# Performance work log

Hardware: AMD Instinct MI355X
Metric: run time of the kernel (lower is better)

## Reference

```python
import jax, jax.numpy as jnp
import numpy as np

N = 50000      # nodes
E = 800000     # edges (avg degree 16)
HID = 64       # hidden_dim
NH = 4         # heads
HC = HID // NH # channels per head = 16
EMB = 8        # emb_dim
EDIM = 6       # edge_dim
SDIM = 6       # state_dim
FEAT = 7       # raw node feature width
NSENS = 3


def setup_inputs() -> dict:
    key = jax.random.key(0)
    k = jax.random.split(key, 32)
    s = 0.1
    p = {}
    p['x'] = jax.random.normal(k[0], (N, FEAT), jnp.float32)
    p['node_type'] = jax.random.randint(k[1], (N,), 0, 2)
    p['sensor_id'] = jax.random.randint(k[2], (N,), 0, NSENS + 1)
    p['edge_index'] = jax.random.randint(k[3], (2, E), 0, N)
    p['edge_attr'] = jax.random.normal(k[4], (E, EDIM), jnp.float32)
    p['hidden_state'] = jnp.zeros((N, HID), jnp.float32)
    # embeddings
    p['type_emb'] = jax.random.normal(k[5], (2, EMB)) * s
    p['sensor_emb'] = jax.random.normal(k[6], (NSENS + 1, EMB)) * s
    # encoder MLP
    p['enc_w1'] = jax.random.normal(k[7], (FEAT + 2 * EMB, HID)) * s
    p['enc_b1'] = jnp.zeros((HID,))
    p['enc_w2'] = jax.random.normal(k[8], (HID, HID)) * s
    p['enc_b2'] = jnp.zeros((HID,))
    # GATv2 layer 1 (lin_l, lin_r with bias; lin_edge no bias; att [NH,HC]; out bias)
    p['g1_wl'] = jax.random.normal(k[9], (HID, HID)) * s
    p['g1_bl'] = jnp.zeros((HID,))
    p['g1_wr'] = jax.random.normal(k[10], (HID, HID)) * s
    p['g1_br'] = jnp.zeros((HID,))
    p['g1_we'] = jax.random.normal(k[11], (EDIM, HID)) * s
    p['g1_att'] = jax.random.normal(k[12], (NH, HC)) * s
    p['g1_bias'] = jnp.zeros((HID,))
    # GATv2 layer 2
    p['g2_wl'] = jax.random.normal(k[13], (HID, HID)) * s
    p['g2_bl'] = jnp.zeros((HID,))
    p['g2_wr'] = jax.random.normal(k[14], (HID, HID)) * s
    p['g2_br'] = jnp.zeros((HID,))
    p['g2_we'] = jax.random.normal(k[15], (EDIM, HID)) * s
    p['g2_att'] = jax.random.normal(k[16], (NH, HC)) * s
    p['g2_bias'] = jnp.zeros((HID,))
    # GRUCell (torch layout transposed: [in, 3*hid], gate order r,z,n)
    p['gru_wih'] = jax.random.normal(k[17], (HID, 3 * HID)) * s
    p['gru_bih'] = jnp.zeros((3 * HID,))
    p['gru_whh'] = jax.random.normal(k[18], (HID, 3 * HID)) * s
    p['gru_bhh'] = jnp.zeros((3 * HID,))
    # decoder MLP
    p['dec_w1'] = jax.random.normal(k[19], (HID, HID)) * s
    p['dec_b1'] = jnp.zeros((HID,))
    p['dec_w2'] = jax.random.normal(k[20], (HID, SDIM + 1)) * s
    p['dec_b2'] = jnp.zeros((SDIM + 1,))
    return p


def _gatv2(h, src, dst, edge_attr, wl, bl, wr, br, we, att, bias):
    # PyG GATv2Conv, concat=True, negative_slope=0.2, edge_dim features
    xl = (h @ wl + bl).reshape(-1, NH, HC)  # source transform [N,H,C]
    xr = (h @ wr + br).reshape(-1, NH, HC)  # target transform [N,H,C]
    xe = (edge_attr @ we).reshape(-1, NH, HC)  # edge transform [E,H,C]
    m = jax.nn.leaky_relu(xl[src] + xr[dst] + xe, 0.2)  # [E,H,C]
    logits = jnp.einsum('ehc,hc->eh', m, att)  # [E,H]
    # scatter-softmax over incoming edges of each destination node
    mx = jax.ops.segment_max(logits, dst, num_segments=N)
    ex = jnp.exp(logits - mx[dst])
    den = jax.ops.segment_sum(ex, dst, num_segments=N)
    alpha = ex / (den[dst] + 1e-16)  # [E,H]
    out = jax.ops.segment_sum(xl[src] * alpha[:, :, None], dst, num_segments=N)
    return out.reshape(-1, NH * HC) + bias, alpha


def reference(x, node_type, sensor_id, edge_index, edge_attr, hidden_state,
              type_emb, sensor_emb, enc_w1, enc_b1, enc_w2, enc_b2,
              g1_wl, g1_bl, g1_wr, g1_br, g1_we, g1_att, g1_bias,
              g2_wl, g2_bl, g2_wr, g2_br, g2_we, g2_att, g2_bias,
              gru_wih, gru_bih, gru_whh, gru_bhh,
              dec_w1, dec_b1, dec_w2, dec_b2):
    src, dst = edge_index[0], edge_index[1]
    h = jnp.concatenate([x, type_emb[node_type], sensor_emb[sensor_id]], axis=-1)
    h = jax.nn.relu(h @ enc_w1 + enc_b1) @ enc_w2 + enc_b2
    h, alpha1 = _gatv2(h, src, dst, edge_attr, g1_wl, g1_bl, g1_wr, g1_br, g1_we, g1_att, g1_bias)
    h = jax.nn.relu(h)
    h, alpha2 = _gatv2(h, src, dst, edge_attr, g2_wl, g2_bl, g2_wr, g2_br, g2_we, g2_att, g2_bias)
    # GRUCell (torch gate order: r, z, n)
    gi = h @ gru_wih + gru_bih
    gh = hidden_state @ gru_whh + gru_bhh
    r = jax.nn.sigmoid(gi[:, :HID] + gh[:, :HID])
    z = jax.nn.sigmoid(gi[:, HID:2 * HID] + gh[:, HID:2 * HID])
    n = jnp.tanh(gi[:, 2 * HID:] + r * gh[:, 2 * HID:])
    new_hidden = (1.0 - z) * n + z * hidden_state
    out = jax.nn.relu(new_hidden @ dec_w1 + dec_b1) @ dec_w2 + dec_b2
    return out, new_hidden, alpha1, alpha2
```

## Files before the change

kernel.cpp:

```cpp
#include <hip/hip_runtime.h>
#include <hip/hip_bf16.h>

static constexpr int N_ = 50000;
static constexpr int E_ = 800000;
static constexpr int CAP = 128;


#define GEMM_FMA_BLOCK(AV, W0, W1, ROW)                                              \
      acc[ROW][0]=fmaf(AV,W0.x,acc[ROW][0]); acc[ROW][1]=fmaf(AV,W0.y,acc[ROW][1]);  \
      acc[ROW][2]=fmaf(AV,W0.z,acc[ROW][2]); acc[ROW][3]=fmaf(AV,W0.w,acc[ROW][3]);  \
      acc[ROW][4]=fmaf(AV,W1.x,acc[ROW][4]); acc[ROW][5]=fmaf(AV,W1.y,acc[ROW][5]);  \
      acc[ROW][6]=fmaf(AV,W1.z,acc[ROW][6]); acc[ROW][7]=fmaf(AV,W1.w,acc[ROW][7]);

#define GEMM_KLOOP(KQc)                                                              \
  _Pragma("unroll 1")                                                                \
  for (int kg = 0; kg < (KQc); ++kg) {                                               \
    float4 a0 = At4[kg * 129 + rowb];                                                \
    float4 a1 = At4[kg * 129 + rowb + 32];                                           \
    float4 a2 = At4[kg * 129 + rowb + 64];                                           \
    float4 a3 = At4[kg * 129 + rowb + 96];                                           \
    _Pragma("unroll")                                                                \
    for (int t = 0; t < 4; ++t) {                                                    \
      float4 w0 = *(const float4*)(Wt + (kg * 4 + t) * 64 + j0);                     \
      float4 w1 = *(const float4*)(Wt + (kg * 4 + t) * 64 + j0 + 4);                 \
      float av0 = t==0?a0.x:t==1?a0.y:t==2?a0.z:a0.w;                                \
      float av1 = t==0?a1.x:t==1?a1.y:t==2?a1.z:a1.w;                                \
      float av2 = t==0?a2.x:t==1?a2.y:t==2?a2.z:a2.w;                                \
      float av3 = t==0?a3.x:t==1?a3.y:t==2?a3.z:a3.w;                                \
      GEMM_FMA_BLOCK(av0, w0, w1, 0)                                                 \
      GEMM_FMA_BLOCK(av1, w0, w1, 1)                                                 \
      GEMM_FMA_BLOCK(av2, w0, w1, 2)                                                 \
      GEMM_FMA_BLOCK(av3, w0, w1, 3)                                                 \
    }                                                                                \
  }

#define ACC_INIT(BPTR)                                                               \
  {                                                                                  \
    float4 b0v = *(const float4*)((BPTR) + j0);                                      \
    float4 b1v = *(const float4*)((BPTR) + j0 + 4);                                  \
    _Pragma("unroll")                                                                \
    for (int i = 0; i < 4; ++i) {                                                    \
      acc[i][0]=b0v.x; acc[i][1]=b0v.y; acc[i][2]=b0v.z; acc[i][3]=b0v.w;            \
      acc[i][4]=b1v.x; acc[i][5]=b1v.y; acc[i][6]=b1v.z; acc[i][7]=b1v.w;            \
    }                                                                                \
  }

#define STAGE_W(WPTR, LDW, KPADc, KREAL)                                             \
  for (int idx = tid; idx < (KPADc) * 16; idx += 256) {                              \
    int k = idx >> 4, jq = idx & 15;                                                 \
    float4 v = (k < (KREAL)) ? *(const float4*)((WPTR) + (size_t)k * (LDW) + jq * 4) \
                             : make_float4(0.f, 0.f, 0.f, 0.f);                      \
    *(float4*)(Wt + k * 64 + jq * 4) = v;                                            \
  }

#define STAGE_A(APTR, LDA, KQc)                                                      \
  for (int idx = tid; idx < 128 * (KQc); idx += 256) {                               \
    int r = idx / (KQc), kq = idx - r * (KQc);                                       \
    int node = nb + r;                                                               \
    float4 v = (node < N_) ? *(const float4*)((APTR) + (size_t)node * (LDA) + kq * 4)\
                           : make_float4(0.f, 0.f, 0.f, 0.f);                        \
    At4[kq * 129 + r] = v;                                                           \
  }

#define STORE_C(CPTR, LDC, RELUc, ACCc)                                              \
  _Pragma("unroll")                                                                  \
  for (int i = 0; i < 4; ++i) {                                                      \
    int node = nb + rowb + 32 * i;                                                   \
    if (node < N_) {                                                                 \
      float* cp = (CPTR) + (size_t)node * (LDC) + j0;                                \
      float o0=acc[i][0],o1=acc[i][1],o2=acc[i][2],o3=acc[i][3];                     \
      float o4=acc[i][4],o5=acc[i][5],o6=acc[i][6],o7=acc[i][7];                     \
      if (RELUc) { o0=fmaxf(o0,0.f);o1=fmaxf(o1,0.f);o2=fmaxf(o2,0.f);o3=fmaxf(o3,0.f); \
                   o4=fmaxf(o4,0.f);o5=fmaxf(o5,0.f);o6=fmaxf(o6,0.f);o7=fmaxf(o7,0.f); } \
      if (ACCc) { float4 c0=*(const float4*)cp; float4 c1=*(const float4*)(cp+4);    \
                  o0+=c0.x;o1+=c0.y;o2+=c0.z;o3+=c0.w;o4+=c1.x;o5+=c1.y;o6+=c1.z;o7+=c1.w; } \
      *(float4*)cp = make_float4(o0,o1,o2,o3);                                       \
      *(float4*)(cp+4) = make_float4(o4,o5,o6,o7);                                   \
    }                                                                                \
  }

__global__ void k_hist(const int* __restrict__ ei, int* __restrict__ deg) {
  int e = blockIdx.x * blockDim.x + threadIdx.x;
  if (e < E_) atomicAdd(&deg[ei[E_ + e]], 1);
}

__global__ __launch_bounds__(1024) void k_scan_blk(const int* __restrict__ deg,
                                                   int* __restrict__ off,
                                                   int* __restrict__ bsum) {
  __shared__ int sm[1024];
  int t = threadIdx.x;
  int i = blockIdx.x * 1024 + t;
  int v = (i < N_) ? deg[i] : 0;
  sm[t] = v;
  __syncthreads();
  for (int s = 1; s < 1024; s <<= 1) {
    int u = (t >= s) ? sm[t - s] : 0;
    __syncthreads();
    sm[t] += u;
    __syncthreads();
  }
  if (i < N_) off[i] = sm[t] - v;
  if (t == 1023) bsum[blockIdx.x] = sm[t];
}

__global__ void k_scan_top(int* __restrict__ bsum, int nb) {
  int t = threadIdx.x;
  int v = (t < nb) ? bsum[t] : 0;
  int orig = v;
  for (int s = 1; s < 64; s <<= 1) {
    int u = __shfl_up(v, s);
    if (t >= s) v += u;
  }
  if (t < nb) bsum[t] = v - orig;
}

__global__ void k_scan_add(int* __restrict__ off, const int* __restrict__ bsum,
                           int* __restrict__ cur) {
  int i = blockIdx.x * blockDim.x + threadIdx.x;
  if (i < N_) {
    int o = off[i] + bsum[i >> 10];
    off[i] = o;
    cur[i] = o;
  }
  if (i == 0) off[N_] = E_;
}

__global__ void k_scatter(const int* __restrict__ ei, int* __restrict__ cursor,
                          int2* __restrict__ csr_es) {
  int e = blockIdx.x * blockDim.x + threadIdx.x;
  if (e < E_) {
    int s = ei[e];
    int d = ei[E_ + e];
    int p = atomicAdd(&cursor[d], 1);
    csr_es[p] = make_int2(e, s);
  }
}

__device__ __forceinline__ float encval(int c, int node, int nt, int sd,
                                        const float* __restrict__ x,
                                        const float* __restrict__ temb,
                                        const float* __restrict__ semb) {
  if (c < 7) return x[node * 7 + c];
  if (c < 15) return temb[nt * 8 + c - 7];
  if (c < 23) return semb[sd * 8 + c - 15];
  return 0.f;
}

__global__ __launch_bounds__(256, 3) void k_gemm_enc(
    const float* __restrict__ x, const int* __restrict__ ntype, const int* __restrict__ sid,
    const float* __restrict__ temb, const float* __restrict__ semb,
    const float* __restrict__ w1, const float* __restrict__ b1,
    float* __restrict__ hout) {
  __shared__ float4 At4[6 * 129];
  __shared__ float Wt[24 * 64];
  int tid = threadIdx.x;
  int nb = blockIdx.x * 128;
  for (int idx = tid; idx < 128 * 6; idx += 256) {
    int r = idx / 6, kq = idx - r * 6;
    int node = nb + r;
    float v0 = 0.f, v1 = 0.f, v2 = 0.f, v3 = 0.f;
    if (node < N_) {
      int nt = ntype[node], sd = sid[node];
      int c = kq * 4;
      v0 = encval(c, node, nt, sd, x, temb, semb);
      v1 = encval(c + 1, node, nt, sd, x, temb, semb);
      v2 = encval(c + 2, node, nt, sd, x, temb, semb);
      v3 = encval(c + 3, node, nt, sd, x, temb, semb);
    }
    At4[kq * 129 + r] = make_float4(v0, v1, v2, v3);
  }
  STAGE_W(w1, 64, 24, 23)
  __syncthreads();
  int col = tid & 7, rowb = tid >> 3;
  int j0 = col * 8;
  float acc[4][8];
  ACC_INIT(b1)
  GEMM_KLOOP(6)
  STORE_C(hout, 64, true, false)
}

__global__ __launch_bounds__(256, 3) void k_gemm64(
    const float* __restrict__ A, const float* __restrict__ W,
    const float* __restrict__ bias, float* __restrict__ C) {
  __shared__ float4 At4[16 * 129];
  __shared__ float Wt[64 * 64];
  int tid = threadIdx.x;
  int nb = blockIdx.x * 128;
  STAGE_A(A, 64, 16)
  STAGE_W(W, 64, 64, 64)
  __syncthreads();
  int col = tid & 7, rowb = tid >> 3;
  int j0 = col * 8;
  float acc[4][8];
  ACC_INIT(bias)
  GEMM_KLOOP(16)
  STORE_C(C, 64, false, false)
}

__global__ __launch_bounds__(256, 3) void k_gemm2(
    const float* __restrict__ A,
    const float* __restrict__ Wl, const float* __restrict__ bl,
    const float* __restrict__ Wr, const float* __restrict__ br,
    float* __restrict__ Cl, float* __restrict__ Cr) {
  __shared__ float4 At4[16 * 129];
  __shared__ float Wt[64 * 64];
  int tid = threadIdx.x;
  int nb = blockIdx.x * 128;
  const float* W = blockIdx.y ? Wr : Wl;
  const float* b = blockIdx.y ? br : bl;
  float* C       = blockIdx.y ? Cr : Cl;
  STAGE_A(A, 64, 16)
  STAGE_W(W, 64, 64, 64)
  __syncthreads();
  int col = tid & 7, rowb = tid >> 3;
  int j0 = col * 8;
  float acc[4][8];
  ACC_INIT(b)
  GEMM_KLOOP(16)
  STORE_C(C, 64, false, false)
}

__global__ __launch_bounds__(256, 3) void k_gru_ih(
    const float* __restrict__ A,
    const float* __restrict__ wih, const float* __restrict__ bih,
    float* __restrict__ gbuf) {
  __shared__ float4 At4[16 * 129];
  __shared__ float Wt[64 * 64];
  int tid = threadIdx.x;
  int nb = blockIdx.x * 128;
  int ch = blockIdx.y;
  int col = tid & 7, rowb = tid >> 3;
  int j0 = col * 8;
  STAGE_A(A, 64, 16)
  STAGE_W(wih + ch * 64, 192, 64, 64)
  __syncthreads();
  float acc[4][8];
  ACC_INIT(bih + ch * 64)
  GEMM_KLOOP(16)
  STORE_C(gbuf + ch * 64, 192, false, false)
}

__global__ __launch_bounds__(256, 3) void k_gru_hh(
    const float* __restrict__ hs,
    const float* __restrict__ whh, const float* __restrict__ bhh,
    float* __restrict__ gbuf, float* __restrict__ outnh) {
  __shared__ float4 At4[16 * 129];
  __shared__ float Wt[64 * 64];
  int tid = threadIdx.x;
  int nb = blockIdx.x * 128;
  int col = tid & 7, rowb = tid >> 3;
  int j0 = col * 8;
  STAGE_A(hs, 64, 16)
  float acc[4][8];
  for (int ch = 0; ch < 3; ++ch) {
    __syncthreads();
    STAGE_W(whh + ch * 64, 192, 64, 64)
    __syncthreads();
    ACC_INIT(bhh + ch * 64)
    GEMM_KLOOP(16)
    if (ch < 2) { STORE_C(gbuf + ch * 64, 192, false, true) }
  }
#define GATE1(RU, ZU, NU, SU, AU, OUT)                                   \
  { float rr = 1.f / (1.f + __expf(-(RU)));                              \
    float zz = 1.f / (1.f + __expf(-(ZU)));                              \
    float nn = tanhf((NU) + rr * (AU));                                  \
    OUT = (1.f - zz) * nn + zz * (SU); }
#pragma unroll
  for (int i = 0; i < 4; ++i) {
    int node = nb + rowb + 32 * i;
    if (node < N_) {
      const float* gp = gbuf + (size_t)node * 192;
      float4 r0 = *(const float4*)(gp + j0);
      float4 r1 = *(const float4*)(gp + j0 + 4);
      float4 z0 = *(const float4*)(gp + 64 + j0);
      float4 z1 = *(const float4*)(gp + 64 + j0 + 4);
      float4 n0 = *(const float4*)(gp + 128 + j0);
      float4 n1 = *(const float4*)(gp + 128 + j0 + 4);
      float4 s0 = *(const float4*)(hs + (size_t)node * 64 + j0);
      float4 s1 = *(const float4*)(hs + (size_t)node * 64 + j0 + 4);
      float q0, q1, q2, q3, q4, q5, q6, q7;
      GATE1(r0.x, z0.x, n0.x, s0.x, acc[i][0], q0)
      GATE1(r0.y, z0.y, n0.y, s0.y, acc[i][1], q1)
      GATE1(r0.z, z0.z, n0.z, s0.z, acc[i][2], q2)
      GATE1(r0.w, z0.w, n0.w, s0.w, acc[i][3], q3)
      GATE1(r1.x, z1.x, n1.x, s1.x, acc[i][4], q4)
      GATE1(r1.y, z1.y, n1.y, s1.y, acc[i][5], q5)
      GATE1(r1.z, z1.z, n1.z, s1.z, acc[i][6], q6)
      GATE1(r1.w, z1.w, n1.w, s1.w, acc[i][7], q7)
      float* op = outnh + (size_t)node * 64 + j0;
      *(float4*)op = make_float4(q0, q1, q2, q3);
      *(float4*)(op + 4) = make_float4(q4, q5, q6, q7);
    }
  }
#undef GATE1
}

__global__ __launch_bounds__(256, 3) void k_dec(
    const float* __restrict__ A,
    const float* __restrict__ w1, const float* __restrict__ b1,
    const float* __restrict__ w2, const float* __restrict__ b2,
    float* __restrict__ out) {
  __shared__ __align__(16) float pool[8320];
  __shared__ float Wt[64 * 64];
  float4* At4 = (float4*)pool;
  float* dtile = pool;
  int tid = threadIdx.x;
  int nb = blockIdx.x * 128;
  STAGE_A(A, 64, 16)
  STAGE_W(w1, 64, 64, 64)
  __syncthreads();
  int col = tid & 7, rowb = tid >> 3;
  int j0 = col * 8;
  float acc[4][8];
  ACC_INIT(b1)
  GEMM_KLOOP(16)
  __syncthreads();
#pragma unroll
  for (int i = 0; i < 4; ++i) {
    int rl = rowb + 32 * i;
#pragma unroll
    for (int u = 0; u < 8; ++u) dtile[rl * 65 + j0 + u] = fmaxf(acc[i][u], 0.f);
  }
  __syncthreads();
  if (tid < 128) {
    int node = nb + tid;
    if (node < N_) {
      float o0 = b2[0], o1 = b2[1], o2 = b2[2], o3 = b2[3], o4 = b2[4], o5 = b2[5], o6 = b2[6];
#pragma unroll 1
      for (int k = 0; k < 64; ++k) {
        float xv = dtile[tid * 65 + k];
        o0 = fmaf(xv, w2[k * 7 + 0], o0);
        o1 = fmaf(xv, w2[k * 7 + 1], o1);
        o2 = fmaf(xv, w2[k * 7 + 2], o2);
        o3 = fmaf(xv, w2[k * 7 + 3], o3);
        o4 = fmaf(xv, w2[k * 7 + 4], o4);
        o5 = fmaf(xv, w2[k * 7 + 5], o5);
        o6 = fmaf(xv, w2[k * 7 + 6], o6);
      }
      float* op = out + (size_t)node * 7;
      op[0] = o0; op[1] = o1; op[2] = o2; op[3] = o3; op[4] = o4; op[5] = o5; op[6] = o6;
    }
  }
}

template <bool RELU>
__global__ __launch_bounds__(64, 6) void k_fused(
    const int* __restrict__ off, const int2* __restrict__ csr_es,
    const float* __restrict__ eattr,
    const float* __restrict__ xl, const float* __restrict__ xr,
    const float* __restrict__ we, const float* __restrict__ att,
    const float* __restrict__ bias,
    float* __restrict__ hout, float* __restrict__ alpha) {
  __shared__ float wes[6 * 64];
  __shared__ float exbuf[CAP * 4];
  __shared__ int ebuf[CAP];
  int lane = threadIdx.x & 63;
  int slot = lane >> 4;
  int q = lane & 15;
  int head = q >> 2;
  int sb = slot << 4;
  int v = blockIdx.x;

#pragma unroll
  for (int i = 0; i < 6; ++i) wes[i * 64 + lane] = we[i * 64 + lane];

  int p0 = off[v], p1 = off[v + 1];
  int cnt = p1 - p0;

  float att4[4], b4[4];
#pragma unroll
  for (int r = 0; r < 4; ++r) { att4[r] = att[q * 4 + r]; b4[r] = bias[q * 4 + r]; }

  float4 xr4 = *(const float4*)(xr + (size_t)v * 64 + q * 4);
  float num0 = 0.f, num1 = 0.f, num2 = 0.f, num3 = 0.f, den = 0.f;

  __syncthreads();

  int p = p0 + slot;
  int2 es = (p < p1) ? csr_es[p] : make_int2(0, 0);
  for (int base = 0; base < cnt; base += 4) {
    bool valid = (p0 + base + slot) < p1;
    int e = es.x, s = es.y;
    int pn = p0 + base + 4 + slot;
    int2 esn = (pn < p1) ? csr_es[pn] : make_int2(0, 0);
    float ea = (valid && q < 6) ? eattr[(size_t)e * 6 + q] : 0.f;
    float4 xls = valid ? *(const float4*)(xl + (size_t)s * 64 + q * 4)
                       : make_float4(0.f, 0.f, 0.f, 0.f);
    float m0 = xls.x + xr4.x, m1 = xls.y + xr4.y, m2 = xls.z + xr4.z, m3 = xls.w + xr4.w;
#pragma unroll
    for (int i = 0; i < 6; ++i) {
      float eai = __shfl(ea, sb + i);
      float4 w4 = *(const float4*)(wes + i * 64 + q * 4);
      m0 = fmaf(eai, w4.x, m0);
      m1 = fmaf(eai, w4.y, m1);
      m2 = fmaf(eai, w4.z, m2);
      m3 = fmaf(eai, w4.w, m3);
    }
    m0 = (m0 > 0.f) ? m0 : 0.2f * m0;
    m1 = (m1 > 0.f) ? m1 : 0.2f * m1;
    m2 = (m2 > 0.f) ? m2 : 0.2f * m2;
    m3 = (m3 > 0.f) ? m3 : 0.2f * m3;
    float t = m0 * att4[0];
    t = fmaf(m1, att4[1], t);
    t = fmaf(m2, att4[2], t);
    t = fmaf(m3, att4[3], t);
    t += __shfl_xor(t, 1);
    t += __shfl_xor(t, 2);
    float ex = valid ? __expf(t) : 0.f;
    den += ex;
    num0 = fmaf(xls.x, ex, num0);
    num1 = fmaf(xls.y, ex, num1);
    num2 = fmaf(xls.z, ex, num2);
    num3 = fmaf(xls.w, ex, num3);
    int idx = base + slot;
    if (valid && idx < CAP) {
      if ((lane & 3) == 0) exbuf[idx * 4 + head] = ex;
      if (q == 0) ebuf[idx] = e;
    }
    es = esn;
  }
  num0 += __shfl_xor(num0, 16); num0 += __shfl_xor(num0, 32);
  num1 += __shfl_xor(num1, 16); num1 += __shfl_xor(num1, 32);
  num2 += __shfl_xor(num2, 16); num2 += __shfl_xor(num2, 32);
  num3 += __shfl_xor(num3, 16); num3 += __shfl_xor(num3, 32);
  den  += __shfl_xor(den, 16);  den  += __shfl_xor(den, 32);
  float dinv = 1.f / (den + 1e-16f);
  float o0 = fmaf(num0, dinv, b4[0]);
  float o1 = fmaf(num1, dinv, b4[1]);
  float o2 = fmaf(num2, dinv, b4[2]);
  float o3 = fmaf(num3, dinv, b4[3]);
  if (RELU) {
    o0 = fmaxf(o0, 0.f); o1 = fmaxf(o1, 0.f); o2 = fmaxf(o2, 0.f); o3 = fmaxf(o3, 0.f);
  }
  if (slot == 0)
    *(float4*)(hout + (size_t)v * 64 + q * 4) = make_float4(o0, o1, o2, o3);
  float dh = __shfl(dinv, (lane & 3) << 2);
  if (cnt <= CAP) {
    for (int base2 = 0; base2 < cnt; base2 += 16) {
      int idx = base2 + (lane >> 2);
      if (idx < cnt) {
        float exv = exbuf[idx * 4 + (lane & 3)];
        int e = ebuf[idx];
        alpha[(size_t)e * 4 + (lane & 3)] = exv * dh;
      }
    }
  } else {
    for (int pp = p0; pp < p1; ++pp) {
      int2 es2 = csr_es[pp];
      int e = es2.x, s = es2.y;
      float ea = (q < 6) ? eattr[(size_t)e * 6 + q] : 0.f;
      float4 xls = *(const float4*)(xl + (size_t)s * 64 + q * 4);
      float m0 = xls.x + xr4.x, m1 = xls.y + xr4.y, m2 = xls.z + xr4.z, m3 = xls.w + xr4.w;
#pragma unroll
      for (int i = 0; i < 6; ++i) {
        float eai = __shfl(ea, i);
        float4 w4 = *(const float4*)(wes + i * 64 + q * 4);
        m0 = fmaf(eai, w4.x, m0);
        m1 = fmaf(eai, w4.y, m1);
        m2 = fmaf(eai, w4.z, m2);
        m3 = fmaf(eai, w4.w, m3);
      }
      m0 = (m0 > 0.f) ? m0 : 0.2f * m0;
      m1 = (m1 > 0.f) ? m1 : 0.2f * m1;
      m2 = (m2 > 0.f) ? m2 : 0.2f * m2;
      m3 = (m3 > 0.f) ? m3 : 0.2f * m3;
      float t = m0 * att4[0];
      t = fmaf(m1, att4[1], t);
      t = fmaf(m2, att4[2], t);
      t = fmaf(m3, att4[3], t);
      t += __shfl_xor(t, 1);
      t += __shfl_xor(t, 2);
      if (slot == 0 && (lane & 3) == 0)
        alpha[(size_t)e * 4 + head] = __expf(t) * dinv;
    }
  }
}

extern "C" void kernel_launch(void* const* d_in, const int* in_sizes, int n_in,
                              void* d_out, int out_size, void* d_ws, size_t ws_size,
                              hipStream_t stream) {
  const float* x      = (const float*)d_in[0];
  const int* ntype    = (const int*)d_in[1];
  const int* sid      = (const int*)d_in[2];
  const int* ei       = (const int*)d_in[3];
  const float* eattr  = (const float*)d_in[4];
  const float* hs     = (const float*)d_in[5];
  const float* temb   = (const float*)d_in[6];
  const float* semb   = (const float*)d_in[7];
  const float* enc_w1 = (const float*)d_in[8];
  const float* enc_b1 = (const float*)d_in[9];
  const float* enc_w2 = (const float*)d_in[10];
  const float* enc_b2 = (const float*)d_in[11];
  const float* g1_wl  = (const float*)d_in[12];
  const float* g1_bl  = (const float*)d_in[13];
  const float* g1_wr  = (const float*)d_in[14];
  const float* g1_br  = (const float*)d_in[15];
  const float* g1_we  = (const float*)d_in[16];
  const float* g1_att = (const float*)d_in[17];
  const float* g1_bias= (const float*)d_in[18];
  const float* g2_wl  = (const float*)d_in[19];
  const float* g2_bl  = (const float*)d_in[20];
  const float* g2_wr  = (const float*)d_in[21];
  const float* g2_br  = (const float*)d_in[22];
  const float* g2_we  = (const float*)d_in[23];
  const float* g2_att = (const float*)d_in[24];
  const float* g2_bias= (const float*)d_in[25];
  const float* gru_wih= (const float*)d_in[26];
  const float* gru_bih= (const float*)d_in[27];
  const float* gru_whh= (const float*)d_in[28];
  const float* gru_bhh= (const float*)d_in[29];
  const float* dec_w1 = (const float*)d_in[30];
  const float* dec_b1 = (const float*)d_in[31];
  const float* dec_w2 = (const float*)d_in[32];
  const float* dec_b2 = (const float*)d_in[33];

  float* ws = (float*)d_ws;
  float* hA = ws;
  float* hB = hA + N_ * 64;
  float* xl = hB + N_ * 64;
  float* xr = xl + N_ * 64;
  float* U  = xr + N_ * 64;
  int* deg  = (int*)(U + N_ * 64);
  int* off  = deg + N_;
  int* cur  = off + N_ + 1;
  int* bsum = cur + N_;
  int2* csr_es = (int2*)(bsum + 64);

  float* gbuf = hB;

  float* out0  = (float*)d_out;
  float* outnh = out0 + N_ * 7;
  float* outa1 = outnh + N_ * 64;
  float* outa2 = outa1 + E_ * 4;

  const int NB_SCAN = (N_ + 1023) / 1024;
  const int NB_GEMM = (N_ + 127) / 128;

  hipMemsetAsync(deg, 0, N_ * sizeof(int), stream);
  k_hist<<<(E_ + 255) / 256, 256, 0, stream>>>(ei, deg);
  k_scan_blk<<<NB_SCAN, 1024, 0, stream>>>(deg, off, bsum);
  k_scan_top<<<1, 64, 0, stream>>>(bsum, NB_SCAN);
  k_scan_add<<<(N_ + 255) / 256, 256, 0, stream>>>(off, bsum, cur);
  k_scatter<<<(E_ + 255) / 256, 256, 0, stream>>>(ei, cur, csr_es);

  k_gemm_enc<<<NB_GEMM, 256, 0, stream>>>(x, ntype, sid, temb, semb, enc_w1, enc_b1, hB);
  k_gemm64<<<NB_GEMM, 256, 0, stream>>>(hB, enc_w2, enc_b2, hA);
  k_gemm2<<<dim3(NB_GEMM, 2), 256, 0, stream>>>(hA, g1_wl, g1_bl, g1_wr, g1_br, xl, xr);
  k_fused<true><<<N_, 64, 0, stream>>>(off, csr_es, eattr, xl, xr,
                                       g1_we, g1_att, g1_bias, hB, outa1);
  k_gemm2<<<dim3(NB_GEMM, 2), 256, 0, stream>>>(hB, g2_wl, g2_bl, g2_wr, g2_br, xl, xr);
  k_fused<false><<<N_, 64, 0, stream>>>(off, csr_es, eattr, xl, xr,
                                        g2_we, g2_att, g2_bias, hA, outa2);
  k_gru_ih<<<dim3(NB_GEMM, 3), 256, 0, stream>>>(hA, gru_wih, gru_bih, gbuf);
  k_gru_hh<<<NB_GEMM, 256, 0, stream>>>(hs, gru_whh, gru_bhh, gbuf, outnh);
  k_dec<<<NB_GEMM, 256, 0, stream>>>(outnh, dec_w1, dec_b1, dec_w2, dec_b2, out0);
}
```

Baseline: 529.0 us.

## Fuse encoder GEMMs and GRU GEMMs, unroll edge loop by two, nontemporal alpha stores

The two encoder GEMMs are merged into one kernel that keeps the ReLU intermediate in shared memory, and the two GRU kernels are merged so the gate preactivations stay in registers instead of going through a global gbuf. The GATv2 edge loop now handles two edge groups per iteration for more memory-level parallelism, and alpha writes use nontemporal stores. This cuts global round trips and launches, at the cost of higher register pressure in the GRU kernel (four 32-float accumulator arrays), which may spill or lower occupancy.

```diff
diff --git a/kernel.cpp b/kernel.cpp
--- a/kernel.cpp
+++ b/kernel.cpp
@@ -146,13 +146,14 @@
   return 0.f;
 }
 
-__global__ __launch_bounds__(256, 3) void k_gemm_enc(
+__global__ __launch_bounds__(256, 3) void k_enc(
     const float* __restrict__ x, const int* __restrict__ ntype, const int* __restrict__ sid,
     const float* __restrict__ temb, const float* __restrict__ semb,
     const float* __restrict__ w1, const float* __restrict__ b1,
+    const float* __restrict__ w2, const float* __restrict__ b2,
     float* __restrict__ hout) {
-  __shared__ float4 At4[6 * 129];
-  __shared__ float Wt[24 * 64];
+  __shared__ float4 At4[16 * 129];
+  __shared__ float Wt[64 * 64];
   int tid = threadIdx.x;
   int nb = blockIdx.x * 128;
   for (int idx = tid; idx < 128 * 6; idx += 256) {
@@ -176,25 +177,22 @@
   float acc[4][8];
   ACC_INIT(b1)
   GEMM_KLOOP(6)
-  STORE_C(hout, 64, true, false)
-}
-
-__global__ __launch_bounds__(256, 3) void k_gemm64(
-    const float* __restrict__ A, const float* __restrict__ W,
-    const float* __restrict__ bias, float* __restrict__ C) {
-  __shared__ float4 At4[16 * 129];
-  __shared__ float Wt[64 * 64];
-  int tid = threadIdx.x;
-  int nb = blockIdx.x * 128;
-  STAGE_A(A, 64, 16)
-  STAGE_W(W, 64, 64, 64)
-  __syncthreads();
-  int col = tid & 7, rowb = tid >> 3;
-  int j0 = col * 8;
-  float acc[4][8];
-  ACC_INIT(bias)
+  __syncthreads();
+#pragma unroll
+  for (int i = 0; i < 4; ++i) {
+    int rl = rowb + 32 * i;
+    At4[(col * 2) * 129 + rl] =
+        make_float4(fmaxf(acc[i][0], 0.f), fmaxf(acc[i][1], 0.f),
+                    fmaxf(acc[i][2], 0.f), fmaxf(acc[i][3], 0.f));
+    At4[(col * 2 + 1) * 129 + rl] =
+        make_float4(fmaxf(acc[i][4], 0.f), fmaxf(acc[i][5], 0.f),
+                    fmaxf(acc[i][6], 0.f), fmaxf(acc[i][7], 0.f));
+  }
+  STAGE_W(w2, 64, 64, 64)
+  __syncthreads();
+  ACC_INIT(b2)
   GEMM_KLOOP(16)
-  STORE_C(C, 64, false, false)
+  STORE_C(hout, 64, false, false)
 }
 
 __global__ __launch_bounds__(256, 3) void k_gemm2(
@@ -220,79 +218,79 @@
   STORE_C(C, 64, false, false)
 }
 
-__global__ __launch_bounds__(256, 3) void k_gru_ih(
-    const float* __restrict__ A,
+__global__ __launch_bounds__(256, 3) void k_gru(
+    const float* __restrict__ hA, const float* __restrict__ hs,
     const float* __restrict__ wih, const float* __restrict__ bih,
-    float* __restrict__ gbuf) {
-  __shared__ float4 At4[16 * 129];
-  __shared__ float Wt[64 * 64];
-  int tid = threadIdx.x;
-  int nb = blockIdx.x * 128;
-  int ch = blockIdx.y;
-  int col = tid & 7, rowb = tid >> 3;
-  int j0 = col * 8;
-  STAGE_A(A, 64, 16)
-  STAGE_W(wih + ch * 64, 192, 64, 64)
-  __syncthreads();
-  float acc[4][8];
-  ACC_INIT(bih + ch * 64)
-  GEMM_KLOOP(16)
-  STORE_C(gbuf + ch * 64, 192, false, false)
-}
-
-__global__ __launch_bounds__(256, 3) void k_gru_hh(
-    const float* __restrict__ hs,
     const float* __restrict__ whh, const float* __restrict__ bhh,
-    float* __restrict__ gbuf, float* __restrict__ outnh) {
+    float* __restrict__ outnh) {
   __shared__ float4 At4[16 * 129];
   __shared__ float Wt[64 * 64];
   int tid = threadIdx.x;
   int nb = blockIdx.x * 128;
   int col = tid & 7, rowb = tid >> 3;
   int j0 = col * 8;
+  float g0[4][8], g1[4][8], g2[4][8];
+  STAGE_A(hA, 64, 16)
+  STAGE_W(wih + 0, 192, 64, 64)
+  __syncthreads();
+  { auto& acc = g0; ACC_INIT(bih + 0) GEMM_KLOOP(16) }
+  __syncthreads();
+  STAGE_W(wih + 64, 192, 64, 64)
+  __syncthreads();
+  { auto& acc = g1; ACC_INIT(bih + 64) GEMM_KLOOP(16) }
+  __syncthreads();
+  STAGE_W(wih + 128, 192, 64, 64)
+  __syncthreads();
+  { auto& acc = g2; ACC_INIT(bih + 128) GEMM_KLOOP(16) }
+  __syncthreads();
   STAGE_A(hs, 64, 16)
-  float acc[4][8];
-  for (int ch = 0; ch < 3; ++ch) {
-    __syncthreads();
-    STAGE_W(whh + ch * 64, 192, 64, 64)
-    __syncthreads();
-    ACC_INIT(bhh + ch * 64)
-    GEMM_KLOOP(16)
-    if (ch < 2) { STORE_C(gbuf + ch * 64, 192, false, true) }
-  }
-#define GATE1(RU, ZU, NU, SU, AU, OUT)                                   \
-  { float rr = 1.f / (1.f + __expf(-(RU)));                              \
-    float zz = 1.f / (1.f + __expf(-(ZU)));                              \
-    float nn = tanhf((NU) + rr * (AU));                                  \
-    OUT = (1.f - zz) * nn + zz * (SU); }
+  STAGE_W(whh + 0, 192, 64, 64)
+  __syncthreads();
+  float gh[4][8];
+  { auto& acc = gh; ACC_INIT(bhh + 0) GEMM_KLOOP(16) }
+#pragma unroll
+  for (int i = 0; i < 4; ++i)
+#pragma unroll
+    for (int u = 0; u < 8; ++u)
+      g0[i][u] = 1.f / (1.f + __expf(-(g0[i][u] + gh[i][u])));
+  __syncthreads();
+  STAGE_W(whh + 64, 192, 64, 64)
+  __syncthreads();
+  { auto& acc = gh; ACC_INIT(bhh + 64) GEMM_KLOOP(16) }
+#pragma unroll
+  for (int i = 0; i < 4; ++i)
+#pragma unroll
+    for (int u = 0; u < 8; ++u)
+      g1[i][u] = 1.f / (1.f + __expf(-(g1[i][u] + gh[i][u])));
+  __syncthreads();
+  STAGE_W(whh + 128, 192, 64, 64)
+  __syncthreads();
+  { auto& acc = gh; ACC_INIT(bhh + 128) GEMM_KLOOP(16) }
+#pragma unroll
+  for (int i = 0; i < 4; ++i)
+#pragma unroll
+    for (int u = 0; u < 8; ++u)
+      g2[i][u] = tanhf(g2[i][u] + g0[i][u] * gh[i][u]);
 #pragma unroll
   for (int i = 0; i < 4; ++i) {
     int node = nb + rowb + 32 * i;
     if (node < N_) {
-      const float* gp = gbuf + (size_t)node * 192;
-      float4 r0 = *(const float4*)(gp + j0);
-      float4 r1 = *(const float4*)(gp + j0 + 4);
-      float4 z0 = *(const float4*)(gp + 64 + j0);
-      float4 z1 = *(const float4*)(gp + 64 + j0 + 4);
-      float4 n0 = *(const float4*)(gp + 128 + j0);
-      float4 n1 = *(const float4*)(gp + 128 + j0 + 4);
-      float4 s0 = *(const float4*)(hs + (size_t)node * 64 + j0);
-      float4 s1 = *(const float4*)(hs + (size_t)node * 64 + j0 + 4);
-      float q0, q1, q2, q3, q4, q5, q6, q7;
-      GATE1(r0.x, z0.x, n0.x, s0.x, acc[i][0], q0)
-      GATE1(r0.y, z0.y, n0.y, s0.y, acc[i][1], q1)
-      GATE1(r0.z, z0.z, n0.z, s0.z, acc[i][2], q2)
-      GATE1(r0.w, z0.w, n0.w, s0.w, acc[i][3], q3)
-      GATE1(r1.x, z1.x, n1.x, s1.x, acc[i][4], q4)
-      GATE1(r1.y, z1.y, n1.y, s1.y, acc[i][5], q5)
-      GATE1(r1.z, z1.z, n1.z, s1.z, acc[i][6], q6)
-      GATE1(r1.w, z1.w, n1.w, s1.w, acc[i][7], q7)
+      int rl = rowb + 32 * i;
+      float4 s0 = At4[(col * 2) * 129 + rl];
+      float4 s1 = At4[(col * 2 + 1) * 129 + rl];
+      float q0 = (1.f - g1[i][0]) * g2[i][0] + g1[i][0] * s0.x;
+      float q1 = (1.f - g1[i][1]) * g2[i][1] + g1[i][1] * s0.y;
+      float q2 = (1.f - g1[i][2]) * g2[i][2] + g1[i][2] * s0.z;
+      float q3 = (1.f - g1[i][3]) * g2[i][3] + g1[i][3] * s0.w;
+      float q4 = (1.f - g1[i][4]) * g2[i][4] + g1[i][4] * s1.x;
+      float q5 = (1.f - g1[i][5]) * g2[i][5] + g1[i][5] * s1.y;
+      float q6 = (1.f - g1[i][6]) * g2[i][6] + g1[i][6] * s1.z;
+      float q7 = (1.f - g1[i][7]) * g2[i][7] + g1[i][7] * s1.w;
       float* op = outnh + (size_t)node * 64 + j0;
       *(float4*)op = make_float4(q0, q1, q2, q3);
       *(float4*)(op + 4) = make_float4(q4, q5, q6, q7);
     }
   }
-#undef GATE1
 }
 
 __global__ __launch_bounds__(256, 3) void k_dec(
@@ -343,6 +341,38 @@
   }
 }
 
+#define EDGE_STEP(XLS, EA, VALID, IDXBASE, EIDX)                                     \
+  { float m0 = XLS.x + xr4.x, m1 = XLS.y + xr4.y;                                    \
+    float m2 = XLS.z + xr4.z, m3 = XLS.w + xr4.w;                                    \
+    _Pragma("unroll")                                                                \
+    for (int i = 0; i < 6; ++i) {                                                    \
+      float eai = __shfl(EA, sb + i);                                                \
+      float4 w4 = *(const float4*)(wes + i * 64 + q * 4);                            \
+      m0 = fmaf(eai, w4.x, m0); m1 = fmaf(eai, w4.y, m1);                            \
+      m2 = fmaf(eai, w4.z, m2); m3 = fmaf(eai, w4.w, m3);                            \
+    }                                                                                \
+    m0 = (m0 > 0.f) ? m0 : 0.2f * m0;                                                \
+    m1 = (m1 > 0.f) ? m1 : 0.2f * m1;                                                \
+    m2 = (m2 > 0.f) ? m2 : 0.2f * m2;                                                \
+    m3 = (m3 > 0.f) ? m3 : 0.2f * m3;                                                \
+    float t = m0 * att4[0];                                                          \
+    t = fmaf(m1, att4[1], t);                                                        \
+    t = fmaf(m2, att4[2], t);                                                        \
+    t = fmaf(m3, att4[3], t);                                                        \
+    t += __shfl_xor(t, 1);                                                           \
+    t += __shfl_xor(t, 2);                                                           \
+    float ex = (VALID) ? __expf(t) : 0.f;                                            \
+    den += ex;                                                                       \
+    num0 = fmaf(XLS.x, ex, num0);                                                    \
+    num1 = fmaf(XLS.y, ex, num1);                                                    \
+    num2 = fmaf(XLS.z, ex, num2);                                                    \
+    num3 = fmaf(XLS.w, ex, num3);                                                    \
+    int idx = (IDXBASE) + slot;                                                      \
+    if ((VALID) && idx < CAP) {                                                      \
+      if ((lane & 3) == 0) exbuf[idx * 4 + head] = ex;                               \
+      if (q == 0) ebuf[idx] = (EIDX);                                                \
+    } }
+
 template <bool RELU>
 __global__ __launch_bounds__(64, 6) void k_fused(
     const int* __restrict__ off, const int2* __restrict__ csr_es,
@@ -376,48 +406,24 @@
 
   __syncthreads();
 
-  int p = p0 + slot;
-  int2 es = (p < p1) ? csr_es[p] : make_int2(0, 0);
-  for (int base = 0; base < cnt; base += 4) {
-    bool valid = (p0 + base + slot) < p1;
-    int e = es.x, s = es.y;
-    int pn = p0 + base + 4 + slot;
-    int2 esn = (pn < p1) ? csr_es[pn] : make_int2(0, 0);
-    float ea = (valid && q < 6) ? eattr[(size_t)e * 6 + q] : 0.f;
-    float4 xls = valid ? *(const float4*)(xl + (size_t)s * 64 + q * 4)
-                       : make_float4(0.f, 0.f, 0.f, 0.f);
-    float m0 = xls.x + xr4.x, m1 = xls.y + xr4.y, m2 = xls.z + xr4.z, m3 = xls.w + xr4.w;
-#pragma unroll
-    for (int i = 0; i < 6; ++i) {
-      float eai = __shfl(ea, sb + i);
-      float4 w4 = *(const float4*)(wes + i * 64 + q * 4);
-      m0 = fmaf(eai, w4.x, m0);
-      m1 = fmaf(eai, w4.y, m1);
-      m2 = fmaf(eai, w4.z, m2);
-      m3 = fmaf(eai, w4.w, m3);
-    }
-    m0 = (m0 > 0.f) ? m0 : 0.2f * m0;
-    m1 = (m1 > 0.f) ? m1 : 0.2f * m1;
-    m2 = (m2 > 0.f) ? m2 : 0.2f * m2;
-    m3 = (m3 > 0.f) ? m3 : 0.2f * m3;
-    float t = m0 * att4[0];
-    t = fmaf(m1, att4[1], t);
-    t = fmaf(m2, att4[2], t);
-    t = fmaf(m3, att4[3], t);
-    t += __shfl_xor(t, 1);
-    t += __shfl_xor(t, 2);
-    float ex = valid ? __expf(t) : 0.f;
-    den += ex;
-    num0 = fmaf(xls.x, ex, num0);
-    num1 = fmaf(xls.y, ex, num1);
-    num2 = fmaf(xls.z, ex, num2);
-    num3 = fmaf(xls.w, ex, num3);
-    int idx = base + slot;
-    if (valid && idx < CAP) {
-      if ((lane & 3) == 0) exbuf[idx * 4 + head] = ex;
-      if (q == 0) ebuf[idx] = e;
-    }
-    es = esn;
+  int2 esA = (p0 + slot < p1) ? csr_es[p0 + slot] : make_int2(0, 0);
+  int2 esB = (p0 + 4 + slot < p1) ? csr_es[p0 + 4 + slot] : make_int2(0, 0);
+  for (int base = 0; base < cnt; base += 8) {
+    int pnA = p0 + base + 8 + slot;
+    int pnB = p0 + base + 12 + slot;
+    int2 esnA = (pnA < p1) ? csr_es[pnA] : make_int2(0, 0);
+    int2 esnB = (pnB < p1) ? csr_es[pnB] : make_int2(0, 0);
+    bool vA = (p0 + base + slot) < p1;
+    bool vB = (p0 + base + 4 + slot) < p1;
+    float eaA = (vA && q < 6) ? eattr[(size_t)esA.x * 6 + q] : 0.f;
+    float eaB = (vB && q < 6) ? eattr[(size_t)esB.x * 6 + q] : 0.f;
+    float4 xlsA = vA ? *(const float4*)(xl + (size_t)esA.y * 64 + q * 4)
+                     : make_float4(0.f, 0.f, 0.f, 0.f);
+    float4 xlsB = vB ? *(const float4*)(xl + (size_t)esB.y * 64 + q * 4)
+                     : make_float4(0.f, 0.f, 0.f, 0.f);
+    EDGE_STEP(xlsA, eaA, vA, base, esA.x)
+    EDGE_STEP(xlsB, eaB, vB, base + 4, esB.x)
+    esA = esnA; esB = esnB;
   }
   num0 += __shfl_xor(num0, 16); num0 += __shfl_xor(num0, 32);
   num1 += __shfl_xor(num1, 16); num1 += __shfl_xor(num1, 32);
@@ -441,7 +447,7 @@
       if (idx < cnt) {
         float exv = exbuf[idx * 4 + (lane & 3)];
         int e = ebuf[idx];
-        alpha[(size_t)e * 4 + (lane & 3)] = exv * dh;
+        __builtin_nontemporal_store(exv * dh, &alpha[(size_t)e * 4 + (lane & 3)]);
       }
     }
   } else {
@@ -471,7 +477,7 @@
       t += __shfl_xor(t, 1);
       t += __shfl_xor(t, 2);
       if (slot == 0 && (lane & 3) == 0)
-        alpha[(size_t)e * 4 + head] = __expf(t) * dinv;
+        __builtin_nontemporal_store(__expf(t) * dinv, &alpha[(size_t)e * 4 + head]);
     }
   }
 }
@@ -526,8 +532,6 @@
   int* bsum = cur + N_;
   int2* csr_es = (int2*)(bsum + 64);
 
-  float* gbuf = hB;
-
   float* out0  = (float*)d_out;
   float* outnh = out0 + N_ * 7;
   float* outa1 = outnh + N_ * 64;
@@ -543,15 +547,14 @@
   k_scan_add<<<(N_ + 255) / 256, 256, 0, stream>>>(off, bsum, cur);
   k_scatter<<<(E_ + 255) / 256, 256, 0, stream>>>(ei, cur, csr_es);
 
-  k_gemm_enc<<<NB_GEMM, 256, 0, stream>>>(x, ntype, sid, temb, semb, enc_w1, enc_b1, hB);
-  k_gemm64<<<NB_GEMM, 256, 0, stream>>>(hB, enc_w2, enc_b2, hA);
+  k_enc<<<NB_GEMM, 256, 0, stream>>>(x, ntype, sid, temb, semb,
+                                     enc_w1, enc_b1, enc_w2, enc_b2, hA);
   k_gemm2<<<dim3(NB_GEMM, 2), 256, 0, stream>>>(hA, g1_wl, g1_bl, g1_wr, g1_br, xl, xr);
   k_fused<true><<<N_, 64, 0, stream>>>(off, csr_es, eattr, xl, xr,
                                        g1_we, g1_att, g1_bias, hB, outa1);
   k_gemm2<<<dim3(NB_GEMM, 2), 256, 0, stream>>>(hB, g2_wl, g2_bl, g2_wr, g2_br, xl, xr);
   k_fused<false><<<N_, 64, 0, stream>>>(off, csr_es, eattr, xl, xr,
                                         g2_we, g2_att, g2_bias, hA, outa2);
-  k_gru_ih<<<dim3(NB_GEMM, 3), 256, 0, stream>>>(hA, gru_wih, gru_bih, gbuf);
-  k_gru_hh<<<NB_GEMM, 256, 0, stream>>>(hs, gru_whh, gru_bhh, gbuf, outnh);
+  k_gru<<<NB_GEMM, 256, 0, stream>>>(hA, hs, gru_wih, gru_bih, gru_whh, gru_bhh, outnh);
   k_dec<<<NB_GEMM, 256, 0, stream>>>(outnh, dec_w1, dec_b1, dec_w2, dec_b2, out0);
 }
```

Measured after the change: 579.1 us. 9.5% more time.
